# Kernel tuning notes

Measured on AMD Instinct MI355X. Metric: run time of the kernel, lower is better.

The kernel has to match this reference:

```python
import jax, jax.numpy as jnp
import numpy as np

NUM_GRAPHS = 100_000
NODES_PER_GRAPH = 38
NUM_NODES = NUM_GRAPHS * NODES_PER_GRAPH
NUM_EDGES = 60_800_000


def setup_inputs() -> dict:
    key = jax.random.key(0)
    ks = jax.random.split(key, 12)
    x = jax.random.normal(ks[0], (NUM_NODES, 1), dtype=jnp.float32)
    edge_index = jax.random.randint(ks[1], (2, NUM_EDGES), 0, NUM_NODES, dtype=jnp.int32)
    edge_attr = jax.random.normal(ks[2], (NUM_EDGES, 1), dtype=jnp.float32)
    # NNConv(1, 1, Linear(1, 1), aggr='add') params
    conv_root = jax.random.normal(ks[3], (1, 1), dtype=jnp.float32)
    conv_bias = jax.random.normal(ks[4], (1,), dtype=jnp.float32) * 0.1
    edge_nn_w = jax.random.normal(ks[5], (1, 1), dtype=jnp.float32)
    edge_nn_b = jax.random.normal(ks[6], (1,), dtype=jnp.float32) * 0.1
    # dense head params: 38 -> 4 -> 4 -> 1
    W1 = jax.random.normal(ks[7], (38, 4), dtype=jnp.float32) * (1.0 / np.sqrt(38))
    b1 = jax.random.normal(ks[8], (4,), dtype=jnp.float32) * 0.1
    W2 = jax.random.normal(ks[9], (4, 4), dtype=jnp.float32) * 0.5
    b2 = jax.random.normal(ks[10], (4,), dtype=jnp.float32) * 0.1
    W3 = jax.random.normal(ks[11], (4, 1), dtype=jnp.float32) * 0.5
    b3 = jnp.zeros((1,), dtype=jnp.float32)
    return {"x": x, "edge_index": edge_index, "edge_attr": edge_attr,
            "conv_root": conv_root, "conv_bias": conv_bias,
            "edge_nn_w": edge_nn_w, "edge_nn_b": edge_nn_b,
            "W1": W1, "b1": b1, "W2": W2, "b2": b2, "W3": W3, "b3": b3}


def reference(x, edge_index, edge_attr, conv_root, conv_bias,
              edge_nn_w, edge_nn_b, W1, b1, W2, b2, W3, b3):
    src, dst = edge_index[0], edge_index[1]  # messages flow src -> dst
    # edge-conditioned weight: Linear(1,1) on edge_attr -> [E,1] (in*out = 1)
    w_e = edge_attr @ edge_nn_w + edge_nn_b            # [E, 1]
    msg = x[src] * w_e                                  # gather + per-edge scale, [E, 1]
    agg = jax.ops.segment_sum(msg, dst, num_segments=NUM_NODES)  # scatter-add, [N, 1]
    nodes = x @ conv_root + agg + conv_bias             # [N, 1]
    h = nodes.reshape(NUM_GRAPHS, NODES_PER_GRAPH)      # [G, 38]
    h = jax.nn.relu(h @ W1 + b1)
    h = jax.nn.relu(h @ W2 + b2)
    out = jax.nn.sigmoid(h @ W3 + b3) * 11.0            # [G, 1]
    return out
```

## Files before the change

### kernel.cpp

```cpp
#include <hip/hip_runtime.h>
#include <hip/hip_fp16.h>
#include <math.h>

constexpr int NG  = 100000;
constexpr int NPG = 38;
constexpr int NN  = NG * NPG;
constexpr long long NE = 60800000LL;

constexpr int BIN_SHIFT = 14;
constexpr int BINW      = 1 << BIN_SHIFT;
constexpr int NB        = (NN + BINW - 1) / BINW;

constexpr int NR    = 4;
constexpr int I4_R  = (int)(NE / 4 / NR);
constexpr int NBLK1 = 1000;
constexpr int I4_B  = I4_R / NBLK1;
constexpr int CHUNK = 4096;
constexpr int CH_I4 = CHUNK / 4;

constexpr int CAPS1 = 68096;
constexpr int CAPD  = 267264;
constexpr int NB2   = 4;
constexpr int NSPLIT = 4;

constexpr size_t AGG_BYTES  = (size_t)NN * 4;
constexpr size_t XH_OFF     = AGG_BYTES;
constexpr size_t XH_BYTES   = (size_t)NB * BINW * 2;
constexpr size_t CUR1_OFF   = XH_OFF + XH_BYTES;
constexpr size_t CUR2_OFF   = CUR1_OFF + 1024;
constexpr size_t PSTRIDE    = (size_t)NB * BINW;
constexpr size_t PART_OFF   = ((CUR2_OFF + 1024 + 255) / 256) * 256;
constexpr size_t PART_BYTES = (size_t)NSPLIT * PSTRIDE * 4;
constexpr size_t REG1_OFF   = PART_OFF + PART_BYTES;
constexpr size_t REG1_BYTES = (size_t)NB * CAPS1 * 8;
constexpr size_t REG2_OFF   = REG1_OFF + REG1_BYTES;
constexpr size_t REG2_BYTES = (size_t)NB * CAPD * 4;
constexpr size_t WS_NEEDED  = REG2_OFF + REG2_BYTES;

__global__ void __launch_bounds__(256) xcast_kernel(
    const float* __restrict__ x, __half2* __restrict__ xh2)
{
    const int i = blockIdx.x * 256 + threadIdx.x;
    if (i < NN / 4) {
        float4 v = ((const float4*)x)[i];
        xh2[2 * i + 0] = __floats2half2_rn(v.x, v.y);
        xh2[2 * i + 1] = __floats2half2_rn(v.z, v.w);
    }
}

__global__ void __launch_bounds__(512) p1_kernel(
    const int*   __restrict__ ei,
    const float* __restrict__ ea,
    const float* __restrict__ wptr,
    const float* __restrict__ bptr,
    unsigned long long* __restrict__ reg1,
    int* __restrict__ cur1,
    int roff)
{
    __shared__ unsigned long long sbuf[CHUNK];
    __shared__ unsigned char     sbin[CHUNK];
    __shared__ int s_scan[256];
    __shared__ int gofs[NB];

    const int t = threadIdx.x;
    if (t < 256) s_scan[t] = 0;
    __syncthreads();

    const float w = wptr[0], b = bptr[0];
    const int4*   src4 = (const int4*)ei + roff + (size_t)blockIdx.x * I4_B;
    const int4*   dst4 = (const int4*)(ei + NE) + roff + (size_t)blockIdx.x * I4_B;
    const float4* ea4  = (const float4*)ea + roff + (size_t)blockIdx.x * I4_B;

    for (int c0 = 0; c0 < I4_B; c0 += CH_I4) {
        const int n4 = min(CH_I4, I4_B - c0);
        int rbin[8]; unsigned long long rpk[8]; int rpos[8];
        #pragma unroll
        for (int u = 0; u < 2; ++u) {
            const int j = u * 512 + t;
            const bool act = j < n4;
            int4   s4 = act ? src4[c0 + j] : make_int4(0, 0, 0, 0);
            int4   d4 = act ? dst4[c0 + j] : make_int4(0, 0, 0, 0);
            float4 e4 = act ? ea4[c0 + j]  : make_float4(0.f, 0.f, 0.f, 0.f);
            int   ss[4] = {s4.x, s4.y, s4.z, s4.w};
            int   dd[4] = {d4.x, d4.y, d4.z, d4.w};
            float ee[4] = {e4.x, e4.y, e4.z, e4.w};
            #pragma unroll
            for (int k = 0; k < 4; ++k) {
                const int idx = u * 4 + k;
                if (act) {
                    const int bin = ss[k] >> BIN_SHIFT;
                    __half_raw hr = __float2half_rn(ee[k] * w + b);
                    rbin[idx] = bin;
                    rpk[idx]  = ((unsigned long long)(unsigned)(ss[k] & (BINW - 1)) << 38)
                              | ((unsigned long long)(unsigned)dd[k] << 16)
                              | (unsigned long long)(unsigned short)hr.x;
                    rpos[idx] = atomicAdd(&s_scan[bin], 1);
                } else { rbin[idx] = -1; rpk[idx] = 0; rpos[idx] = 0; }
            }
        }
        __syncthreads();

        int acc = 0;
        if (t < 256) acc = s_scan[t];
        for (int off = 1; off < 256; off <<= 1) {
            int tmp = 0;
            if (t < 256 && t >= off) tmp = s_scan[t - off];
            __syncthreads();
            if (t < 256) { acc += tmp; s_scan[t] = acc; }
            __syncthreads();
        }

        if (t < NB) {
            const int excl = (t == 0) ? 0 : s_scan[t - 1];
            const int rl   = s_scan[t] - excl;
            gofs[t] = (rl > 0) ? atomicAdd(&cur1[t], rl) : 0;
        }
        #pragma unroll
        for (int k = 0; k < 8; ++k) {
            if (rbin[k] >= 0) {
                const int excl = (rbin[k] == 0) ? 0 : s_scan[rbin[k] - 1];
                const int idx  = excl + rpos[k];
                sbuf[idx] = rpk[k];
                sbin[idx] = (unsigned char)rbin[k];
            }
        }
        __syncthreads();

        const int tot = n4 * 4;
        for (int k = t; k < tot; k += 512) {
            const unsigned long long r = sbuf[k];
            const int bin  = sbin[k];
            const int excl = (bin == 0) ? 0 : s_scan[bin - 1];
            reg1[(size_t)bin * CAPS1 + gofs[bin] + (k - excl)] = r;
        }
        __syncthreads();
        if (t < 256) s_scan[t] = 0;
        __syncthreads();
    }
}

__global__ void __launch_bounds__(512) p2_kernel(
    const __half* __restrict__ xh,
    const unsigned long long* __restrict__ reg1,
    const int* __restrict__ cur1,
    unsigned int* __restrict__ reg2,
    int* __restrict__ cur2)
{
    __shared__ __half        xsl[BINW];
    __shared__ unsigned int  sbuf[CHUNK];
    __shared__ unsigned char sbin[CHUNK];
    __shared__ int s_scan[256];
    __shared__ int gofs[NB];

    const int t  = threadIdx.x;
    const int sb = blockIdx.x >> 2;
    const int jb = blockIdx.x & 3;

    {
        const uint4* s = (const uint4*)(xh + (size_t)sb * BINW);
        uint4* d = (uint4*)xsl;
        for (int i = t; i < BINW / 8; i += 512) d[i] = s[i];
    }
    if (t < 256) s_scan[t] = 0;
    __syncthreads();

    const int n2    = cur1[sb];
    const int cpb   = (n2 + NB2 - 1) / NB2;
    const int start = jb * cpb;
    const int end   = min(start + cpb, n2);
    const unsigned long long* seg = reg1 + (size_t)sb * CAPS1;

    for (int c0 = start; c0 < end; c0 += CHUNK) {
        const int cnt = min(CHUNK, end - c0);
        int rbin[8]; unsigned int rpk[8]; int rpos[8];
        #pragma unroll
        for (int u = 0; u < 8; ++u) {
            const int j = u * 512 + t;
            if (j < cnt) {
                const unsigned long long r = seg[c0 + j];
                const int srclow        = (int)(r >> 38);
                const unsigned int dst  = (unsigned int)(r >> 16) & 0x3FFFFFu;
                __half_raw hm; hm.x = (unsigned short)(r & 0xFFFFu);
                const float msg = __half2float(xsl[srclow]) * __half2float(__half(hm));
                __half_raw ho = __float2half_rn(msg);
                const int bin = (int)(dst >> BIN_SHIFT);
                rbin[u] = bin;
                rpk[u]  = ((dst & (unsigned)(BINW - 1)) << 16) | (unsigned int)(unsigned short)ho.x;
                rpos[u] = atomicAdd(&s_scan[bin], 1);
            } else { rbin[u] = -1; rpk[u] = 0; rpos[u] = 0; }
        }
        __syncthreads();

        int acc = 0;
        if (t < 256) acc = s_scan[t];
        for (int off = 1; off < 256; off <<= 1) {
            int tmp = 0;
            if (t < 256 && t >= off) tmp = s_scan[t - off];
            __syncthreads();
            if (t < 256) { acc += tmp; s_scan[t] = acc; }
            __syncthreads();
        }

        if (t < NB) {
            const int excl = (t == 0) ? 0 : s_scan[t - 1];
            const int rl   = s_scan[t] - excl;
            gofs[t] = (rl > 0) ? atomicAdd(&cur2[t], rl) : 0;
        }
        #pragma unroll
        for (int u = 0; u < 8; ++u) {
            if (rbin[u] >= 0) {
                const int excl = (rbin[u] == 0) ? 0 : s_scan[rbin[u] - 1];
                const int idx  = excl + rpos[u];
                sbuf[idx] = rpk[u];
                sbin[idx] = (unsigned char)rbin[u];
            }
        }
        __syncthreads();

        for (int k = t; k < cnt; k += 512) {
            const unsigned int r = sbuf[k];
            const int bin  = sbin[k];
            const int excl = (bin == 0) ? 0 : s_scan[bin - 1];
            reg2[(size_t)bin * CAPD + gofs[bin] + (k - excl)] = r;
        }
        __syncthreads();
        if (t < 256) s_scan[t] = 0;
        __syncthreads();
    }
}

__global__ void __launch_bounds__(512) reduce_kernel(
    const unsigned int* __restrict__ reg2,
    const int* __restrict__ cur2,
    float* __restrict__ part_agg)
{
    __shared__ float acc[BINW];
    const int t    = threadIdx.x;
    const int b    = blockIdx.x / NSPLIT;
    const int part = blockIdx.x % NSPLIT;
    for (int i = t; i < BINW; i += 512) acc[i] = 0.0f;
    __syncthreads();

    const int n  = cur2[b];
    const int i0 = (int)(((long long)part * n) / NSPLIT);
    const int i1 = (int)(((long long)(part + 1) * n) / NSPLIT);
    const unsigned int* seg = reg2 + (size_t)b * CAPD;

    int k = i0 + t;
    for (; k + 3584 < i1; k += 4096) {
        unsigned int r[8];
        #pragma unroll
        for (int u = 0; u < 8; ++u) r[u] = seg[k + u * 512];
        #pragma unroll
        for (int u = 0; u < 8; ++u) {
            __half_raw h; h.x = (unsigned short)(r[u] & 0xFFFFu);
            atomicAdd(&acc[r[u] >> 16], __half2float(__half(h)));
        }
    }
    for (; k < i1; k += 512) {
        unsigned int r = seg[k];
        __half_raw h; h.x = (unsigned short)(r & 0xFFFFu);
        atomicAdd(&acc[r >> 16], __half2float(__half(h)));
    }
    __syncthreads();

    float* dst = part_agg + (size_t)part * PSTRIDE + ((size_t)b << BIN_SHIFT);
    for (int i = t; i < BINW; i += 512) dst[i] = acc[i];
}

__global__ void __launch_bounds__(256) combine_kernel(
    const float* __restrict__ part_agg, float* __restrict__ agg)
{
    const int stride = gridDim.x * 256;
    const int n4 = NN / 4;
    const float4* p0 = (const float4*)(part_agg);
    const float4* p1 = (const float4*)(part_agg + PSTRIDE);
    const float4* p2 = (const float4*)(part_agg + 2 * PSTRIDE);
    const float4* p3 = (const float4*)(part_agg + 3 * PSTRIDE);
    float4* o = (float4*)agg;
    for (int i = blockIdx.x * 256 + threadIdx.x; i < n4; i += stride) {
        float4 a = p0[i], b = p1[i], c = p2[i], d = p3[i];
        float4 r;
        r.x = a.x + b.x + c.x + d.x;
        r.y = a.y + b.y + c.y + d.y;
        r.z = a.z + b.z + c.z + d.z;
        r.w = a.w + b.w + c.w + d.w;
        o[i] = r;
    }
}

__global__ void __launch_bounds__(256) edge_kernel(
    const float* __restrict__ x,
    const int*   __restrict__ ei,
    const float* __restrict__ ea,
    const float* __restrict__ wptr,
    const float* __restrict__ bptr,
    float*       __restrict__ agg)
{
    const float w = wptr[0];
    const float b = bptr[0];
    const int nvec = (int)(NE / 4);
    const int4*   src4 = (const int4*)ei;
    const int4*   dst4 = (const int4*)(ei + NE);
    const float4* ea4  = (const float4*)ea;
    const int stride = gridDim.x * blockDim.x;
    for (int i = blockIdx.x * blockDim.x + threadIdx.x; i < nvec; i += stride) {
        int4   s = src4[i];
        int4   d = dst4[i];
        float4 e = ea4[i];
        atomicAdd(&agg[d.x], x[s.x] * (e.x * w + b));
        atomicAdd(&agg[d.y], x[s.y] * (e.y * w + b));
        atomicAdd(&agg[d.z], x[s.z] * (e.z * w + b));
        atomicAdd(&agg[d.w], x[s.w] * (e.w * w + b));
    }
}

__global__ void __launch_bounds__(256) head_kernel(
    const float* __restrict__ x,
    const float* __restrict__ agg,
    const float* __restrict__ conv_root,
    const float* __restrict__ conv_bias,
    const float* __restrict__ W1, const float* __restrict__ b1,
    const float* __restrict__ W2, const float* __restrict__ b2,
    const float* __restrict__ W3, const float* __restrict__ b3,
    float* __restrict__ out)
{
    __shared__ float nv[256 * NPG];
    const float cr = conv_root[0];
    const float cb = conv_bias[0];

    const int gbase = blockIdx.x * 256;
    const int gcount = (NG - gbase < 256) ? (NG - gbase) : 256;
    const int fcount = gcount * NPG;
    const long long nbase = (long long)gbase * NPG;

    for (int k = threadIdx.x; k < fcount; k += 256) {
        long long gi = nbase + k;
        nv[k] = x[gi] * cr + agg[gi] + cb;
    }
    __syncthreads();

    const int g = gbase + threadIdx.x;
    if (g < NG) {
        const float* p = &nv[threadIdx.x * NPG];
        float h0 = b1[0], h1 = b1[1], h2 = b1[2], h3 = b1[3];
        #pragma unroll
        for (int j = 0; j < NPG; ++j) {
            float v = p[j];
            h0 += v * W1[j * 4 + 0];
            h1 += v * W1[j * 4 + 1];
            h2 += v * W1[j * 4 + 2];
            h3 += v * W1[j * 4 + 3];
        }
        h0 = fmaxf(h0, 0.f); h1 = fmaxf(h1, 0.f);
        h2 = fmaxf(h2, 0.f); h3 = fmaxf(h3, 0.f);

        float q0 = b2[0] + h0 * W2[0] + h1 * W2[4] + h2 * W2[8]  + h3 * W2[12];
        float q1 = b2[1] + h0 * W2[1] + h1 * W2[5] + h2 * W2[9]  + h3 * W2[13];
        float q2 = b2[2] + h0 * W2[2] + h1 * W2[6] + h2 * W2[10] + h3 * W2[14];
        float q3 = b2[3] + h0 * W2[3] + h1 * W2[7] + h2 * W2[11] + h3 * W2[15];
        q0 = fmaxf(q0, 0.f); q1 = fmaxf(q1, 0.f);
        q2 = fmaxf(q2, 0.f); q3 = fmaxf(q3, 0.f);

        float z = b3[0] + q0 * W3[0] + q1 * W3[1] + q2 * W3[2] + q3 * W3[3];
        float sgm = 1.0f / (1.0f + __expf(-z));
        out[g] = 11.0f * sgm;
    }
}

extern "C" void kernel_launch(void* const* d_in, const int* in_sizes, int n_in,
                              void* d_out, int out_size, void* d_ws, size_t ws_size,
                              hipStream_t stream) {
    const float* x         = (const float*)d_in[0];
    const int*   ei        = (const int*)  d_in[1];
    const float* ea        = (const float*)d_in[2];
    const float* conv_root = (const float*)d_in[3];
    const float* conv_bias = (const float*)d_in[4];
    const float* ew        = (const float*)d_in[5];
    const float* eb        = (const float*)d_in[6];
    const float* W1        = (const float*)d_in[7];
    const float* b1        = (const float*)d_in[8];
    const float* W2        = (const float*)d_in[9];
    const float* b2        = (const float*)d_in[10];
    const float* W3        = (const float*)d_in[11];
    const float* b3        = (const float*)d_in[12];

    char*  ws  = (char*)d_ws;
    float* agg = (float*)ws;
    float* out = (float*)d_out;

    if (ws_size >= WS_NEEDED) {
        __half*             xh    = (__half*)(ws + XH_OFF);
        int*                cur1  = (int*)(ws + CUR1_OFF);
        int*                cur2  = (int*)(ws + CUR2_OFF);
        float*              partp = (float*)(ws + PART_OFF);
        unsigned long long* reg1  = (unsigned long long*)(ws + REG1_OFF);
        unsigned int*       reg2  = (unsigned int*)(ws + REG2_OFF);

        xcast_kernel<<<(NN / 4 + 255) / 256, 256, 0, stream>>>(x, (__half2*)xh);
        hipMemsetAsync(cur2, 0, NB * sizeof(int), stream);
        for (int r = 0; r < NR; ++r) {
            hipMemsetAsync(cur1, 0, NB * sizeof(int), stream);
            p1_kernel<<<NBLK1, 512, 0, stream>>>(ei, ea, ew, eb, reg1, cur1, r * I4_R);
            p2_kernel<<<NB * NB2, 512, 0, stream>>>(xh, reg1, cur1, reg2, cur2);
        }
        reduce_kernel<<<NB * NSPLIT, 512, 0, stream>>>(reg2, cur2, partp);
        combine_kernel<<<2048, 256, 0, stream>>>(partp, agg);
    } else {
        hipMemsetAsync(agg, 0, AGG_BYTES, stream);
        edge_kernel<<<2048, 256, 0, stream>>>(x, ei, ea, ew, eb, agg);
    }

    const int hblocks = (NG + 255) / 256;
    head_kernel<<<hblocks, 256, 0, stream>>>(x, agg, conv_root, conv_bias,
                                             W1, b1, W2, b2, W3, b3, out);
}
```

Baseline: 1.225 ms.

## Fuse partial-sum combine into head kernel and halve reduce splits with prefetch

The reduce kernel now splits each bin into two halves handled by 1024-thread blocks instead of four parts on 512-thread blocks. Its main loop software-prefetches the next 8 loads while issuing LDS atomics for the current batch. The separate combine kernel is removed, and a new head kernel sums the two partial aggregates directly while building node values. This drops one launch and a full read/write pass over the aggregate array, at the cost of fewer reduce blocks and more registers per thread.

```diff
diff --git a/kernel.cpp b/kernel.cpp
--- a/kernel.cpp
+++ b/kernel.cpp
@@ -21,7 +21,7 @@
 constexpr int CAPS1 = 68096;
 constexpr int CAPD  = 267264;
 constexpr int NB2   = 4;
-constexpr int NSPLIT = 4;
+constexpr int NSPLIT = 2;
 
 constexpr size_t AGG_BYTES  = (size_t)NN * 4;
 constexpr size_t XH_OFF     = AGG_BYTES;
@@ -229,35 +229,48 @@
     }
 }
 
-__global__ void __launch_bounds__(512) reduce_kernel(
+__global__ void __launch_bounds__(1024) reduce_kernel(
     const unsigned int* __restrict__ reg2,
     const int* __restrict__ cur2,
     float* __restrict__ part_agg)
 {
     __shared__ float acc[BINW];
     const int t    = threadIdx.x;
-    const int b    = blockIdx.x / NSPLIT;
-    const int part = blockIdx.x % NSPLIT;
-    for (int i = t; i < BINW; i += 512) acc[i] = 0.0f;
-    __syncthreads();
-
-    const int n  = cur2[b];
-    const int i0 = (int)(((long long)part * n) / NSPLIT);
-    const int i1 = (int)(((long long)(part + 1) * n) / NSPLIT);
+    const int b    = blockIdx.x >> 1;
+    const int part = blockIdx.x & 1;
+    for (int i = t; i < BINW; i += 1024) acc[i] = 0.0f;
+    __syncthreads();
+
+    const int n    = cur2[b];
+    const int half = n >> 1;
+    const int i0   = part ? half : 0;
+    const int i1   = part ? n : half;
     const unsigned int* seg = reg2 + (size_t)b * CAPD;
 
+    unsigned int a[8], nb[8];
     int k = i0 + t;
-    for (; k + 3584 < i1; k += 4096) {
-        unsigned int r[8];
-        #pragma unroll
-        for (int u = 0; u < 8; ++u) r[u] = seg[k + u * 512];
+    if (k + 7168 < i1) {
+        #pragma unroll
+        for (int u = 0; u < 8; ++u) a[u] = seg[k + u * 1024];
+        k += 8192;
+        for (; k + 7168 < i1; k += 8192) {
+            #pragma unroll
+            for (int u = 0; u < 8; ++u) nb[u] = seg[k + u * 1024];
+            #pragma unroll
+            for (int u = 0; u < 8; ++u) {
+                __half_raw h; h.x = (unsigned short)(a[u] & 0xFFFFu);
+                atomicAdd(&acc[a[u] >> 16], __half2float(__half(h)));
+            }
+            #pragma unroll
+            for (int u = 0; u < 8; ++u) a[u] = nb[u];
+        }
         #pragma unroll
         for (int u = 0; u < 8; ++u) {
-            __half_raw h; h.x = (unsigned short)(r[u] & 0xFFFFu);
-            atomicAdd(&acc[r[u] >> 16], __half2float(__half(h)));
-        }
-    }
-    for (; k < i1; k += 512) {
+            __half_raw h; h.x = (unsigned short)(a[u] & 0xFFFFu);
+            atomicAdd(&acc[a[u] >> 16], __half2float(__half(h)));
+        }
+    }
+    for (; k < i1; k += 1024) {
         unsigned int r = seg[k];
         __half_raw h; h.x = (unsigned short)(r & 0xFFFFu);
         atomicAdd(&acc[r >> 16], __half2float(__half(h)));
@@ -265,28 +278,7 @@
     __syncthreads();
 
     float* dst = part_agg + (size_t)part * PSTRIDE + ((size_t)b << BIN_SHIFT);
-    for (int i = t; i < BINW; i += 512) dst[i] = acc[i];
-}
-
-__global__ void __launch_bounds__(256) combine_kernel(
-    const float* __restrict__ part_agg, float* __restrict__ agg)
-{
-    const int stride = gridDim.x * 256;
-    const int n4 = NN / 4;
-    const float4* p0 = (const float4*)(part_agg);
-    const float4* p1 = (const float4*)(part_agg + PSTRIDE);
-    const float4* p2 = (const float4*)(part_agg + 2 * PSTRIDE);
-    const float4* p3 = (const float4*)(part_agg + 3 * PSTRIDE);
-    float4* o = (float4*)agg;
-    for (int i = blockIdx.x * 256 + threadIdx.x; i < n4; i += stride) {
-        float4 a = p0[i], b = p1[i], c = p2[i], d = p3[i];
-        float4 r;
-        r.x = a.x + b.x + c.x + d.x;
-        r.y = a.y + b.y + c.y + d.y;
-        r.z = a.z + b.z + c.z + d.z;
-        r.w = a.w + b.w + c.w + d.w;
-        o[i] = r;
-    }
+    for (int i = t; i < BINW; i += 1024) dst[i] = acc[i];
 }
 
 __global__ void __launch_bounds__(256) edge_kernel(
@@ -312,6 +304,60 @@
         atomicAdd(&agg[d.y], x[s.y] * (e.y * w + b));
         atomicAdd(&agg[d.z], x[s.z] * (e.z * w + b));
         atomicAdd(&agg[d.w], x[s.w] * (e.w * w + b));
+    }
+}
+
+__global__ void __launch_bounds__(256) head_kernel2(
+    const float* __restrict__ x,
+    const float* __restrict__ p0,
+    const float* __restrict__ p1,
+    const float* __restrict__ conv_root,
+    const float* __restrict__ conv_bias,
+    const float* __restrict__ W1, const float* __restrict__ b1,
+    const float* __restrict__ W2, const float* __restrict__ b2,
+    const float* __restrict__ W3, const float* __restrict__ b3,
+    float* __restrict__ out)
+{
+    __shared__ float nv[256 * NPG];
+    const float cr = conv_root[0];
+    const float cb = conv_bias[0];
+
+    const int gbase = blockIdx.x * 256;
+    const int gcount = (NG - gbase < 256) ? (NG - gbase) : 256;
+    const int fcount = gcount * NPG;
+    const long long nbase = (long long)gbase * NPG;
+
+    for (int k = threadIdx.x; k < fcount; k += 256) {
+        long long gi = nbase + k;
+        nv[k] = x[gi] * cr + p0[gi] + p1[gi] + cb;
+    }
+    __syncthreads();
+
+    const int g = gbase + threadIdx.x;
+    if (g < NG) {
+        const float* p = &nv[threadIdx.x * NPG];
+        float h0 = b1[0], h1 = b1[1], h2 = b1[2], h3 = b1[3];
+        #pragma unroll
+        for (int j = 0; j < NPG; ++j) {
+            float v = p[j];
+            h0 += v * W1[j * 4 + 0];
+            h1 += v * W1[j * 4 + 1];
+            h2 += v * W1[j * 4 + 2];
+            h3 += v * W1[j * 4 + 3];
+        }
+        h0 = fmaxf(h0, 0.f); h1 = fmaxf(h1, 0.f);
+        h2 = fmaxf(h2, 0.f); h3 = fmaxf(h3, 0.f);
+
+        float q0 = b2[0] + h0 * W2[0] + h1 * W2[4] + h2 * W2[8]  + h3 * W2[12];
+        float q1 = b2[1] + h0 * W2[1] + h1 * W2[5] + h2 * W2[9]  + h3 * W2[13];
+        float q2 = b2[2] + h0 * W2[2] + h1 * W2[6] + h2 * W2[10] + h3 * W2[14];
+        float q3 = b2[3] + h0 * W2[3] + h1 * W2[7] + h2 * W2[11] + h3 * W2[15];
+        q0 = fmaxf(q0, 0.f); q1 = fmaxf(q1, 0.f);
+        q2 = fmaxf(q2, 0.f); q3 = fmaxf(q3, 0.f);
+
+        float z = b3[0] + q0 * W3[0] + q1 * W3[1] + q2 * W3[2] + q3 * W3[3];
+        float sgm = 1.0f / (1.0f + __expf(-z));
+        out[g] = 11.0f * sgm;
     }
 }
 
@@ -404,14 +450,17 @@
             p1_kernel<<<NBLK1, 512, 0, stream>>>(ei, ea, ew, eb, reg1, cur1, r * I4_R);
             p2_kernel<<<NB * NB2, 512, 0, stream>>>(xh, reg1, cur1, reg2, cur2);
         }
-        reduce_kernel<<<NB * NSPLIT, 512, 0, stream>>>(reg2, cur2, partp);
-        combine_kernel<<<2048, 256, 0, stream>>>(partp, agg);
+        reduce_kernel<<<NB * NSPLIT, 1024, 0, stream>>>(reg2, cur2, partp);
+
+        const int hblocks = (NG + 255) / 256;
+        head_kernel2<<<hblocks, 256, 0, stream>>>(x, partp, partp + PSTRIDE,
+                                                  conv_root, conv_bias,
+                                                  W1, b1, W2, b2, W3, b3, out);
     } else {
         hipMemsetAsync(agg, 0, AGG_BYTES, stream);
         edge_kernel<<<2048, 256, 0, stream>>>(x, ei, ea, ew, eb, agg);
-    }
-
-    const int hblocks = (NG + 255) / 256;
-    head_kernel<<<hblocks, 256, 0, stream>>>(x, agg, conv_root, conv_bias,
-                                             W1, b1, W2, b2, W3, b3, out);
-}
+        const int hblocks = (NG + 255) / 256;
+        head_kernel<<<hblocks, 256, 0, stream>>>(x, agg, conv_root, conv_bias,
+                                                 W1, b1, W2, b2, W3, b3, out);
+    }
+}
```

Result: no change. 1.213 ms (-0.9%).
